# Kernel optimization log

Measured on AMD Instinct MI355X. Metric: run time of the kernel, lower is better.

Reference implementation:

```python
import jax, jax.numpy as jnp
import numpy as np

D = 1024          # d_model
DQ = D // 4       # embedding dim (d_model//4)
DH = D // 2       # head hidden (d_model//2)
P = 6             # n_digit_positions = max_int_digits + n_decimal_digits
NOPS, NPT = 9, 10
B, T = 8, 2048


def _ln(x, g, b, eps=1e-5):
    m = jnp.mean(x, axis=-1, keepdims=True)
    v = jnp.mean(jnp.square(x - m), axis=-1, keepdims=True)
    return (x - m) * jax.lax.rsqrt(v + eps) * g + b


def _xavier(key, shape):
    fan_in, fan_out = shape[-2], shape[-1]
    lim = np.sqrt(6.0 / (fan_in + fan_out))
    return jax.random.uniform(key, shape, jnp.float32, -lim, lim)


def setup_inputs() -> dict:
    key = jax.random.key(0)
    ks = jax.random.split(key, 20)
    inp = {
        'hidden': jax.random.normal(ks[0], (B, T, D), jnp.float32),
        'operation_type': jax.random.randint(ks[1], (B,), 0, NOPS),
        'param_type': jax.random.randint(ks[2], (B, T), 0, NPT),
        # embeddings (std=0.02 like the torch init)
        'op_embed': 0.02 * jax.random.normal(ks[3], (NOPS, DQ), jnp.float32),
        'pt_embed': 0.02 * jax.random.normal(ks[4], (NPT, DQ), jnp.float32),
        'pos_embed': 0.02 * jax.random.normal(ks[5], (P, DQ), jnp.float32),
        # context_proj: Linear(D + D//2 -> D) + LayerNorm(D)
        'ctx_w': _xavier(ks[6], (D + D // 2, D)),
        'ctx_b': jnp.zeros((D,), jnp.float32),
        'ctx_g': jnp.ones((D,), jnp.float32),
        'ctx_beta': jnp.zeros((D,), jnp.float32),
        # sign_head: Linear(D->DH), LN(DH), Linear(DH->3)
        'sign_w1': _xavier(ks[7], (D, DH)),
        'sign_b1': jnp.zeros((DH,), jnp.float32),
        'sign_g': jnp.ones((DH,), jnp.float32),
        'sign_beta': jnp.zeros((DH,), jnp.float32),
        'sign_w2': _xavier(ks[8], (DH, 3)),
        'sign_b2': jnp.zeros((3,), jnp.float32),
        # digit heads stacked over positions: Linear(D+DQ->DH), LN(DH), Linear(DH->10)
        'dig_w1': _xavier(ks[9], (P, D + DQ, DH)),
        'dig_b1': jnp.zeros((P, DH), jnp.float32),
        'dig_g': jnp.ones((P, DH), jnp.float32),
        'dig_beta': jnp.zeros((P, DH), jnp.float32),
        'dig_w2': _xavier(ks[10], (P, DH, 10)),
        'dig_b2': jnp.zeros((P, 10), jnp.float32),
        'aux_w1': _xavier(ks[11], (D, DH)),
        'aux_b1': jnp.zeros((DH,), jnp.float32),
        'aux_w2': _xavier(ks[12], (DH, 1)),
        'aux_b2': jnp.zeros((1,), jnp.float32),
    }
    return inp


def reference(hidden, operation_type, param_type, op_embed, pt_embed, pos_embed,
              ctx_w, ctx_b, ctx_g, ctx_beta,
              sign_w1, sign_b1, sign_g, sign_beta, sign_w2, sign_b2,
              dig_w1, dig_b1, dig_g, dig_beta, dig_w2, dig_b2,
              aux_w1, aux_b1, aux_w2, aux_b2):
    b, t, d = hidden.shape
    gelu = lambda x: jax.nn.gelu(x, approximate=False)  # torch nn.GELU default

    op_emb = jnp.broadcast_to(op_embed[operation_type][:, None, :], (b, t, DQ))
    pm_emb = pt_embed[param_type]                       # [B,T,DQ]
    ctx_in = jnp.concatenate([hidden, op_emb, pm_emb], axis=-1)  # [B,T,1.5D]
    context = gelu(_ln(ctx_in @ ctx_w + ctx_b, ctx_g, ctx_beta))  # [B,T,D]

    sh = gelu(_ln(context @ sign_w1 + sign_b1, sign_g, sign_beta))
    sign_logits = sh @ sign_w2 + sign_b2                # [B,T,3]

    # digit heads, vectorized over position. concat(context, pos_emb[p]) @ W1
    # == context @ W1[:, :D] + pos_emb[p] @ W1[:, D:]
    h = (jnp.einsum('btd,pdh->btph', context, dig_w1[:, :D, :])
         + jnp.einsum('pq,pqh->ph', pos_embed, dig_w1[:, D:, :])
         + dig_b1)                                      # [B,T,P,DH]
    h = gelu(_ln(h, dig_g, dig_beta))
    digit_logits = jnp.einsum('btph,pho->btpo', h, dig_w2) + dig_b2  # [B,T,P,10]

    aux_value = gelu(context @ aux_w1 + aux_b1) @ aux_w2 + aux_b2    # [B,T,1]

    return sign_logits, digit_logits, aux_value
```

## Files before the change

kernel.cpp:

```cpp
#include <hip/hip_runtime.h>
#include <hip/hip_bf16.h>

typedef unsigned short u16;
typedef __attribute__((ext_vector_type(8))) __bf16 bf16x8;
typedef __attribute__((ext_vector_type(4))) float f32x4;

typedef __attribute__((address_space(1))) const void GVoid;
typedef __attribute__((address_space(3))) void LVoid;

__device__ __forceinline__ void async_load16(const u16* g, u16* l) {
    __builtin_amdgcn_global_load_lds((GVoid*)g, (LVoid*)l, 16, 0, 0);
}

__device__ __forceinline__ float bf2f(u16 u) {
    union { unsigned i; float f; } v; v.i = ((unsigned)u) << 16; return v.f;
}
__device__ __forceinline__ u16 f2bf(float f) {
    union { float f; unsigned i; } v; v.f = f;
    unsigned r = (v.i + 0x7FFFu + ((v.i >> 16) & 1u)) >> 16;
    return (u16)r;
}
__device__ __forceinline__ float gelu_f(float x) {
    float t = x * fmaf(0.0356774081f, x * x, 0.7978845608f);
    float e = __expf(2.0f * t);
    float r = 1.0f / (e + 1.0f);
    return x - x * r;
}

#define OP_E   0
#define PT_E   2304
#define POS_E  4864
#define CTX_B  6400
#define CTX_G  7424
#define CTX_BE 8448
#define S_B1   9472
#define S_G    9984
#define S_BE   10496
#define S_B2   11008
#define D_G    11012
#define D_BE   14084
#define D_B2   17156
#define A_B1   17216
#define A_B2   17728

struct SmallTab {
    const float* src[15];
    int off[15];
    int cnt[15];
};

__global__ __launch_bounds__(256) void convert_small(SmallTab tab, u16* __restrict__ dst)
{
    int idx = blockIdx.x * 256 + threadIdx.x;
#pragma unroll
    for (int e = 0; e < 15; ++e) {
        if (idx < tab.cnt[e]) {
            dst[tab.off[e] + idx] = f2bf(tab.src[e][idx]);
            return;
        }
        idx -= tab.cnt[e];
    }
}

__global__ __launch_bounds__(256) void transpose_all(
    const float* __restrict__ ctx_w, const float* __restrict__ sign_w1,
    const float* __restrict__ aux_w1, const float* __restrict__ dig_w1,
    u16* __restrict__ ctxWt, u16* __restrict__ BtAll)
{
    __shared__ u16 tl[32][33];
    int z = blockIdx.z;
    const float* src; u16* dst; size_t srcOff = 0; int srcLd, cols;
    if (z == 8) { src = ctx_w; dst = ctxWt; srcLd = 1024; cols = 1024; }
    else {
        srcLd = 512; cols = 512;
        if (z == 0) src = sign_w1;
        else if (z == 1) src = aux_w1;
        else { src = dig_w1; srcOff = (size_t)(z - 2) * 1280 * 512; }
        dst = BtAll + (size_t)z * 512 * 1024;
    }
    int n0 = blockIdx.x * 32;
    if (n0 >= cols) return;
    int k0 = blockIdx.y * 32;
    int t = threadIdx.x;
    int r = t >> 3;
    int c4 = (t & 7) * 4;
    float4 v = *(const float4*)&src[srcOff + (size_t)(k0 + r) * srcLd + n0 + c4];
    tl[r][c4 + 0] = f2bf(v.x); tl[r][c4 + 1] = f2bf(v.y);
    tl[r][c4 + 2] = f2bf(v.z); tl[r][c4 + 3] = f2bf(v.w);
    __syncthreads();
    ushort4 o;
    o.x = tl[c4 + 0][r]; o.y = tl[c4 + 1][r]; o.z = tl[c4 + 2][r]; o.w = tl[c4 + 3][r];
    *(ushort4*)&dst[(size_t)(n0 + r) * 1024 + k0 + c4] = o;
}

__global__ __launch_bounds__(256) void precompute_bias(
    const float* __restrict__ ctx_w, const float* __restrict__ dig_w1,
    const float* __restrict__ op_embed, const float* __restrict__ pt_embed,
    const float* __restrict__ pos_embed, const float* __restrict__ dig_b1,
    const int* __restrict__ op_type,
    float* __restrict__ E_op, float* __restrict__ P_pt, float* __restrict__ dbias)
{
    int idx = blockIdx.x * 256 + threadIdx.x;
    if (idx < 8192) {
        int b = idx >> 10, n = idx & 1023;
        const float* e = op_embed + op_type[b] * 256;
        float s = 0.f;
        for (int q = 0; q < 256; ++q)
            s += e[q] * ctx_w[(size_t)(1024 + q) * 1024 + n];
        E_op[idx] = s;
    } else if (idx < 18432) {
        int i = idx - 8192;
        int v = i >> 10, n = i & 1023;
        const float* e = pt_embed + v * 256;
        float s = 0.f;
        for (int q = 0; q < 256; ++q)
            s += e[q] * ctx_w[(size_t)(1280 + q) * 1024 + n];
        P_pt[i] = s;
    } else if (idx < 21504) {
        int i = idx - 18432;
        int p = i >> 9, h = i & 511;
        const float* e = pos_embed + p * 256;
        float s = dig_b1[p * 512 + h];
        for (int q = 0; q < 256; ++q)
            s += e[q] * dig_w1[(size_t)p * 1280 * 512 + (size_t)(1024 + q) * 512 + h];
        dbias[i] = s;
    }
}

__global__ __launch_bounds__(256) void build_vec(
    const u16* __restrict__ csm, const float* __restrict__ dbias,
    float* __restrict__ biasAll, float* __restrict__ gammaAll,
    float* __restrict__ betaAll)
{
    int n = blockIdx.x * 256 + threadIdx.x;
    float bi, g, be;
    if (n < 512) {
        bi = bf2f(csm[S_B1 + n]); g = bf2f(csm[S_G + n]); be = bf2f(csm[S_BE + n]);
    } else if (n < 1024) {
        bi = bf2f(csm[A_B1 + n - 512]); g = 1.f; be = 0.f;
    } else {
        int h = n - 1024;
        bi = dbias[h]; g = bf2f(csm[D_G + h]); be = bf2f(csm[D_BE + h]);
    }
    biasAll[n] = bi; gammaAll[n] = g; betaAll[n] = be;
}

__global__ __launch_bounds__(256) void build_w2pad(
    const float* __restrict__ sign_w2, const float* __restrict__ dig_w2,
    const float* __restrict__ aux_w2, u16* __restrict__ W2pad)
{
    int idx = blockIdx.x * 256 + threadIdx.x;
    int row = idx >> 12, k = idx & 4095;
    int r = row >> 4, o = row & 15;
    float v = 0.f;
    if (r == 0) {
        if (o < 3 && k < 512) v = sign_w2[k * 3 + o];
    } else if (r == 7) {
        if (o == 0 && k >= 512 && k < 1024) v = aux_w2[k - 512];
    } else {
        int p = r - 1, lo = 1024 + p * 512;
        if (o < 10 && k >= lo && k < lo + 512) v = dig_w2[(size_t)p * 5120 + (k - lo) * 10 + o];
    }
    W2pad[idx] = f2bf(v);
}

__global__ __launch_bounds__(256) void gemm_bf16(
    const u16* __restrict__ A, const u16* __restrict__ Bt, u16* __restrict__ C,
    int M, int N, int K)
{
    __shared__ u16 As[128 * 32];
    __shared__ u16 Bs[128 * 32];
    const int tid = threadIdx.x;
    const int wid = tid >> 6, lane = tid & 63;
    const int m0 = blockIdx.x * 128, n0 = blockIdx.y * 128;
    const int mw = (wid >> 1) * 64, nw = (wid & 1) * 64;
    const int quad = lane >> 4, r16 = lane & 15;

    f32x4 acc[4][4] = {};

    const int srow = wid * 32 + (lane >> 2);
    const int scol = (lane & 3) * 8;
    const u16* gA = A + (size_t)(m0 + srow) * K + scol;
    const u16* gB = Bt + (size_t)(n0 + srow) * K + scol;
    u16* lA = As + wid * 32 * 32;
    u16* lB = Bs + wid * 32 * 32;

    for (int k0 = 0; k0 < K; k0 += 32) {
        async_load16(gA + k0, lA);
        async_load16(gA + k0 + (size_t)16 * K, lA + 16 * 32);
        async_load16(gB + k0, lB);
        async_load16(gB + k0 + (size_t)16 * K, lB + 16 * 32);
        __syncthreads();
        bf16x8 af[4], bw[4];
#pragma unroll
        for (int i = 0; i < 4; ++i)
            af[i] = *(const bf16x8*)&As[(mw + i * 16 + r16) * 32 + quad * 8];
#pragma unroll
        for (int j = 0; j < 4; ++j)
            bw[j] = *(const bf16x8*)&Bs[(nw + j * 16 + r16) * 32 + quad * 8];
#pragma unroll
        for (int i = 0; i < 4; ++i)
#pragma unroll
            for (int j = 0; j < 4; ++j)
                acc[i][j] = __builtin_amdgcn_mfma_f32_16x16x32_bf16(
                    af[i], bw[j], acc[i][j], 0, 0, 0);
        __syncthreads();
    }

#pragma unroll
    for (int i = 0; i < 4; ++i) {
#pragma unroll
        for (int j = 0; j < 4; ++j) {
            int col = n0 + nw + j * 16 + r16;
            size_t base = (size_t)(m0 + mw + i * 16 + quad * 4) * N + col;
#pragma unroll
            for (int r = 0; r < 4; ++r)
                C[base + (size_t)r * N] = f2bf(acc[i][j][r]);
        }
    }
}

__global__ __launch_bounds__(256) void gemm_f32a(
    const float* __restrict__ A, const u16* __restrict__ Bt, u16* __restrict__ C,
    int M, int N, int K)
{
    __shared__ u16 As[128 * 32];
    __shared__ u16 Bs[128 * 32];
    const int tid = threadIdx.x;
    const int wid = tid >> 6, lane = tid & 63;
    const int m0 = blockIdx.x * 128, n0 = blockIdx.y * 128;
    const int mw = (wid >> 1) * 64, nw = (wid & 1) * 64;
    const int quad = lane >> 4, r16 = lane & 15;

    f32x4 acc[4][4] = {};

    const int srow = wid * 32 + (lane >> 2);
    const int scol = (lane & 3) * 8;
    const u16* gB = Bt + (size_t)(n0 + srow) * K + scol;
    u16* lB = Bs + wid * 32 * 32;

    const int r0 = tid >> 2;
    const int c8 = (tid & 3) * 8;

    for (int k0 = 0; k0 < K; k0 += 32) {
        async_load16(gB + k0, lB);
        async_load16(gB + k0 + (size_t)16 * K, lB + 16 * 32);
        const float* p0 = &A[(size_t)(m0 + r0) * K + k0 + c8];
        const float* p1 = &A[(size_t)(m0 + 64 + r0) * K + k0 + c8];
        float4 x = *(const float4*)p0, y = *(const float4*)(p0 + 4);
        float4 u = *(const float4*)p1, w = *(const float4*)(p1 + 4);
        uint4 a0, a1;
        a0.x = f2bf(x.x) | ((unsigned)f2bf(x.y) << 16);
        a0.y = f2bf(x.z) | ((unsigned)f2bf(x.w) << 16);
        a0.z = f2bf(y.x) | ((unsigned)f2bf(y.y) << 16);
        a0.w = f2bf(y.z) | ((unsigned)f2bf(y.w) << 16);
        a1.x = f2bf(u.x) | ((unsigned)f2bf(u.y) << 16);
        a1.y = f2bf(u.z) | ((unsigned)f2bf(u.w) << 16);
        a1.z = f2bf(w.x) | ((unsigned)f2bf(w.y) << 16);
        a1.w = f2bf(w.z) | ((unsigned)f2bf(w.w) << 16);
        *(uint4*)&As[r0 * 32 + c8] = a0;
        *(uint4*)&As[(64 + r0) * 32 + c8] = a1;
        __syncthreads();

        bf16x8 af[4], bw[4];
#pragma unroll
        for (int i = 0; i < 4; ++i)
            af[i] = *(const bf16x8*)&As[(mw + i * 16 + r16) * 32 + quad * 8];
#pragma unroll
        for (int j = 0; j < 4; ++j)
            bw[j] = *(const bf16x8*)&Bs[(nw + j * 16 + r16) * 32 + quad * 8];
#pragma unroll
        for (int i = 0; i < 4; ++i)
#pragma unroll
            for (int j = 0; j < 4; ++j)
                acc[i][j] = __builtin_amdgcn_mfma_f32_16x16x32_bf16(
                    af[i], bw[j], acc[i][j], 0, 0, 0);
        __syncthreads();
    }

#pragma unroll
    for (int i = 0; i < 4; ++i) {
#pragma unroll
        for (int j = 0; j < 4; ++j) {
            int col = n0 + nw + j * 16 + r16;
            size_t base = (size_t)(m0 + mw + i * 16 + quad * 4) * N + col;
#pragma unroll
            for (int r = 0; r < 4; ++r)
                C[base + (size_t)r * N] = f2bf(acc[i][j][r]);
        }
    }
}

__global__ __launch_bounds__(256) void ln_ctx_kernel(
    const u16* __restrict__ pre, const float* __restrict__ E_op,
    const float* __restrict__ P_pt, const int* __restrict__ ptype,
    const u16* __restrict__ csm, u16* __restrict__ ctx, int tokOff)
{
    __shared__ float red[8];
    int local = blockIdx.x;
    int token = tokOff + local;
    int b = token >> 11;
    int pt = ptype[token];
    int tid = threadIdx.x;
    int c = tid * 4;
    int wid = tid >> 6, lane = tid & 63;

    ushort4 xp = *(const ushort4*)&pre[(size_t)local * 1024 + c];
    float4 eo = *(const float4*)&E_op[b * 1024 + c];
    float4 pp = *(const float4*)&P_pt[pt * 1024 + c];
    ushort4 cb4 = *(const ushort4*)&csm[CTX_B + c];
    float x[4];
    x[0] = bf2f(xp.x) + eo.x + pp.x + bf2f(cb4.x);
    x[1] = bf2f(xp.y) + eo.y + pp.y + bf2f(cb4.y);
    x[2] = bf2f(xp.z) + eo.z + pp.z + bf2f(cb4.z);
    x[3] = bf2f(xp.w) + eo.w + pp.w + bf2f(cb4.w);

    float s = x[0] + x[1] + x[2] + x[3];
    float s2 = x[0]*x[0] + x[1]*x[1] + x[2]*x[2] + x[3]*x[3];
    for (int off = 32; off; off >>= 1) { s += __shfl_xor(s, off); s2 += __shfl_xor(s2, off); }
    if (lane == 0) { red[wid] = s; red[4 + wid] = s2; }
    __syncthreads();
    s  = red[0] + red[1] + red[2] + red[3];
    s2 = red[4] + red[5] + red[6] + red[7];
    float mean = s * (1.f / 1024.f);
    float var = fmaxf(s2 * (1.f / 1024.f) - mean * mean, 0.f);
    float rs = rsqrtf(var + 1e-5f);

    ushort4 g4 = *(const ushort4*)&csm[CTX_G + c];
    ushort4 b4 = *(const ushort4*)&csm[CTX_BE + c];
    ushort4 o;
    o.x = f2bf(gelu_f((x[0] - mean) * rs * bf2f(g4.x) + bf2f(b4.x)));
    o.y = f2bf(gelu_f((x[1] - mean) * rs * bf2f(g4.y) + bf2f(b4.y)));
    o.z = f2bf(gelu_f((x[2] - mean) * rs * bf2f(g4.z) + bf2f(b4.z)));
    o.w = f2bf(gelu_f((x[3] - mean) * rs * bf2f(g4.w) + bf2f(b4.w)));
    *(ushort4*)&ctx[(size_t)token * 1024 + c] = o;
}

__global__ __launch_bounds__(256) void ln_stats(
    const u16* __restrict__ hp, const float* __restrict__ biasAll,
    float2* __restrict__ stats, int Rh)
{
    int wid = threadIdx.x >> 6, lane = threadIdx.x & 63;
    int idx = blockIdx.x * 4 + wid;
    int token = idx >> 3, s = idx & 7;
    const u16* row = hp + (size_t)token * 4096 + s * 512 + lane * 8;
    ushort4 a = ((const ushort4*)row)[0];
    ushort4 b = ((const ushort4*)row)[1];
    u16 xr[8]; *(ushort4*)&xr[0] = a; *(ushort4*)&xr[4] = b;
    const float* bi = biasAll + s * 512 + lane * 8;
    float4 b0 = *(const float4*)bi, b1 = *(const float4*)(bi + 4);
    float bb[8] = {b0.x, b0.y, b0.z, b0.w, b1.x, b1.y, b1.z, b1.w};
    float sm = 0.f, s2 = 0.f;
#pragma unroll
    for (int j = 0; j < 8; ++j) {
        float v = bf2f(xr[j]) + bb[j];
        sm += v; s2 += v * v;
    }
    for (int off = 32; off; off >>= 1) { sm += __shfl_xor(sm, off); s2 += __shfl_xor(s2, off); }
    if (lane == 0) {
        float mean = sm * (1.f / 512.f);
        float var = fmaxf(s2 * (1.f / 512.f) - mean * mean, 0.f);
        float2 st = make_float2(mean, rsqrtf(var + 1e-5f));
        if (s == 1) st = make_float2(0.f, 1.f);
        stats[idx] = st;
    }
}

__global__ __launch_bounds__(256) void gemm_final(
    const u16* __restrict__ A, const u16* __restrict__ W2pad,
    const float* __restrict__ biasAll, const float* __restrict__ gammaAll,
    const float* __restrict__ betaAll, const float2* __restrict__ stats,
    float* __restrict__ out_pre, int Rh)
{
    __shared__ u16 As[128 * 32];
    __shared__ u16 Bs[128 * 32];
    const int tid = threadIdx.x;
    const int wid = tid >> 6, lane = tid & 63;
    const int m0 = blockIdx.x * 128;
    const int ks = blockIdx.y, kbase = ks * 1024;
    const int mw = (wid >> 1) * 64, nw = (wid & 1) * 64;
    const int quad = lane >> 4, r16 = lane & 15;

    f32x4 acc[4][4] = {};

    const int srow = wid * 32 + (lane >> 2);
    const int scol = (lane & 3) * 8;
    const u16* gB = W2pad + (size_t)srow * 4096 + kbase + scol;
    u16* lB = Bs + wid * 32 * 32;

    const int r0 = tid >> 2;
    const int c8 = (tid & 3) * 8;

    for (int k0 = 0; k0 < 1024; k0 += 32) {
        async_load16(gB + k0, lB);
        async_load16(gB + k0 + (size_t)16 * 4096, lB + 16 * 32);
        int kk = kbase + k0 + c8;
        int sl = kk >> 9;
        float4 bi0 = *(const float4*)&biasAll[kk], bi1 = *(const float4*)&biasAll[kk + 4];
        float4 g0 = *(const float4*)&gammaAll[kk], g1 = *(const float4*)&gammaAll[kk + 4];
        float4 be0 = *(const float4*)&betaAll[kk], be1 = *(const float4*)&betaAll[kk + 4];
        float bb[8] = {bi0.x, bi0.y, bi0.z, bi0.w, bi1.x, bi1.y, bi1.z, bi1.w};
        float gg[8] = {g0.x, g0.y, g0.z, g0.w, g1.x, g1.y, g1.z, g1.w};
        float bt[8] = {be0.x, be0.y, be0.z, be0.w, be1.x, be1.y, be1.z, be1.w};
#pragma unroll
        for (int h = 0; h < 2; ++h) {
            int row = m0 + r0 + h * 64;
            const u16* ap = A + (size_t)row * 4096 + kk;
            ushort4 xa = ((const ushort4*)ap)[0];
            ushort4 xb = ((const ushort4*)ap)[1];
            u16 xr[8]; *(ushort4*)&xr[0] = xa; *(ushort4*)&xr[4] = xb;
            float2 st = stats[row * 8 + sl];
            u16 o[8];
#pragma unroll
            for (int j = 0; j < 8; ++j) {
                float v = (bf2f(xr[j]) + bb[j] - st.x) * st.y * gg[j] + bt[j];
                o[j] = f2bf(gelu_f(v));
            }
            *(uint4*)&As[(h * 64 + r0) * 32 + c8] = *(const uint4*)&o[0];
        }
        __syncthreads();

        bf16x8 af[4], bw[4];
#pragma unroll
        for (int i = 0; i < 4; ++i)
            af[i] = *(const bf16x8*)&As[(mw + i * 16 + r16) * 32 + quad * 8];
#pragma unroll
        for (int j = 0; j < 4; ++j)
            bw[j] = *(const bf16x8*)&Bs[(nw + j * 16 + r16) * 32 + quad * 8];
#pragma unroll
        for (int i = 0; i < 4; ++i)
#pragma unroll
            for (int j = 0; j < 4; ++j)
                acc[i][j] = __builtin_amdgcn_mfma_f32_16x16x32_bf16(
                    af[i], bw[j], acc[i][j], 0, 0, 0);
        __syncthreads();
    }

    float* op = out_pre + (size_t)ks * Rh * 128;
#pragma unroll
    for (int i = 0; i < 4; ++i) {
#pragma unroll
        for (int j = 0; j < 4; ++j) {
            int col = nw + j * 16 + r16;
            size_t base = (size_t)(m0 + mw + i * 16 + quad * 4) * 128 + col;
#pragma unroll
            for (int r = 0; r < 4; ++r)
                op[base + (size_t)r * 128] = acc[i][j][r];
        }
    }
}

__global__ __launch_bounds__(256) void gather_out(
    const float* __restrict__ out_pre, const u16* __restrict__ csm,
    float* __restrict__ out, int tokOff, int Rh)
{
    int idx = blockIdx.x * 256 + threadIdx.x;
    if (idx >= Rh * 64) return;
    int local = idx >> 6;
    int c = idx & 63;
    int token = tokOff + local;
    size_t P = (size_t)Rh * 128;
    size_t base = (size_t)local * 128;
    int col;
    if (c < 3) col = c;
    else if (c == 63) col = 7 * 16;
    else { int d = c - 3; int p = d / 10; col = (p + 1) * 16 + (d - p * 10); }
    float v = out_pre[base + col] + out_pre[P + base + col]
            + out_pre[2 * P + base + col] + out_pre[3 * P + base + col];
    if (c < 3) {
        out[(size_t)token * 3 + c] = v + bf2f(csm[S_B2 + c]);
    } else if (c == 63) {
        out[1032192 + (size_t)token] = v + bf2f(csm[A_B2]);
    } else {
        int d = c - 3;
        int p = d / 10, o = d - p * 10;
        out[49152 + ((size_t)token * 6 + p) * 10 + o] = v + bf2f(csm[D_B2 + p * 10 + o]);
    }
}

extern "C" void kernel_launch(void* const* d_in, const int* in_sizes, int n_in,
                              void* d_out, int out_size, void* d_ws, size_t ws_size,
                              hipStream_t stream) {
    const float* hidden    = (const float*)d_in[0];
    const int*   op_type   = (const int*)d_in[1];
    const int*   pt_type   = (const int*)d_in[2];
    const float* op_embed  = (const float*)d_in[3];
    const float* pt_embed  = (const float*)d_in[4];
    const float* pos_embed = (const float*)d_in[5];
    const float* ctx_w     = (const float*)d_in[6];
    const float* sign_w1   = (const float*)d_in[10];
    const float* sign_w2   = (const float*)d_in[14];
    const float* dig_w1    = (const float*)d_in[16];
    const float* dig_b1    = (const float*)d_in[17];
    const float* dig_w2    = (const float*)d_in[20];
    const float* aux_w1    = (const float*)d_in[22];
    const float* aux_w2    = (const float*)d_in[24];

    char* ws = (char*)d_ws;
    u16*    ctxWt    = (u16*)(ws + 0);
    u16*    BtAll    = (u16*)(ws + 2097152);
    float*  E_op     = (float*)(ws + 10485760);
    float*  P_pt     = (float*)(ws + 10518528);
    float*  dbias    = (float*)(ws + 10559488);
    u16*    csm      = (u16*)(ws + 10571776);
    float*  biasAll  = (float*)(ws + 10637312);
    float*  gammaAll = (float*)(ws + 10653696);
    float*  betaAll  = (float*)(ws + 10670080);
    float2* stats    = (float2*)(ws + 10686464);
    u16*    context  = (u16*)(ws + 11735040);
    u16*    scratch  = (u16*)(ws + 45289472);
    u16*    W2pad    = ctxWt;
    size_t S = (ws_size > 45289472) ? ws_size - 45289472 : 0;

    int Rc = 16384;
    while ((size_t)Rc * 2048 > S && Rc > 128) Rc >>= 1;
    int Rh = 16384;
    while ((size_t)Rh * 8192 > S && Rh > 128) Rh >>= 1;

    float* out = (float*)d_out;

    SmallTab tab;
    const float* srcs[15] = { op_embed, pt_embed, pos_embed,
                              (const float*)d_in[7], (const float*)d_in[8], (const float*)d_in[9],
                              (const float*)d_in[11], (const float*)d_in[12], (const float*)d_in[13],
                              (const float*)d_in[15],
                              (const float*)d_in[18], (const float*)d_in[19], (const float*)d_in[21],
                              (const float*)d_in[23], (const float*)d_in[25] };
    const int offs[15] = { OP_E, PT_E, POS_E, CTX_B, CTX_G, CTX_BE,
                           S_B1, S_G, S_BE, S_B2,
                           D_G, D_BE, D_B2, A_B1, A_B2 };
    const int cnts[15] = { 2304, 2560, 1536, 1024, 1024, 1024,
                           512, 512, 512, 3,
                           3072, 3072, 60, 512, 1 };
    for (int i = 0; i < 15; ++i) { tab.src[i] = srcs[i]; tab.off[i] = offs[i]; tab.cnt[i] = cnts[i]; }
    convert_small<<<70, 256, 0, stream>>>(tab, csm);

    transpose_all<<<dim3(32, 32, 9), 256, 0, stream>>>(
        ctx_w, sign_w1, aux_w1, dig_w1, ctxWt, BtAll);
    precompute_bias<<<84, 256, 0, stream>>>(
        ctx_w, dig_w1, op_embed, pt_embed, pos_embed, dig_b1, op_type,
        E_op, P_pt, dbias);
    build_vec<<<16, 256, 0, stream>>>(csm, dbias, biasAll, gammaAll, betaAll);

    for (int t0 = 0; t0 < 16384; t0 += Rc) {
        gemm_f32a<<<dim3(Rc / 128, 8), 256, 0, stream>>>(
            hidden + (size_t)t0 * 1024, ctxWt, scratch, Rc, 1024, 1024);
        ln_ctx_kernel<<<Rc, 256, 0, stream>>>(
            scratch, E_op, P_pt, pt_type, csm, context, t0);
    }

    build_w2pad<<<2048, 256, 0, stream>>>(sign_w2, dig_w2, aux_w2, W2pad);

    for (int t0 = 0; t0 < 16384; t0 += Rh) {
        gemm_bf16<<<dim3(Rh / 128, 32), 256, 0, stream>>>(
            context + (size_t)t0 * 1024, BtAll, scratch, Rh, 4096, 1024);
        ln_stats<<<Rh * 2, 256, 0, stream>>>(scratch, biasAll, stats, Rh);
        float* out_pre = (float*)(context + (size_t)t0 * 1024);
        gemm_final<<<dim3(Rh / 128, 4), 256, 0, stream>>>(
            scratch, W2pad, biasAll, gammaAll, betaAll, stats, out_pre, Rh);
        gather_out<<<(Rh * 64 + 255) / 256, 256, 0, stream>>>(
            out_pre, csm, out, t0, Rh);
    }
}
```

Baseline: 568.7 us.

## Replace head GEMM with 256x256 double-buffered, phase-interleaved MFMA kernel

Replaces the simple 128x128 single-buffered head GEMM with a 512-thread, 256x256-tile kernel that uses 128KB of LDS, a double-buffered K=64 pipeline, XOR-swizzled LDS layout, and four compute phases, each interleaved with async global-to-LDS loads and barriers. It also adds a grid swizzle for L2 locality and raises MFMA priority with setprio. The aim is to hide load latency behind MFMA work and raise arithmetic intensity in the largest GEMM (16384x4096x1024). Costs: hardcoded N=4096 and K=1024, a minimum chunk of 256 rows, and a single block per CU because of the LDS size.

```diff
diff --git a/kernel.cpp b/kernel.cpp
--- a/kernel.cpp
+++ b/kernel.cpp
@@ -164,58 +164,122 @@
     W2pad[idx] = f2bf(v);
 }
 
-__global__ __launch_bounds__(256) void gemm_bf16(
+__global__ __launch_bounds__(512) void gemm_head_8ph(
     const u16* __restrict__ A, const u16* __restrict__ Bt, u16* __restrict__ C,
-    int M, int N, int K)
-{
-    __shared__ u16 As[128 * 32];
-    __shared__ u16 Bs[128 * 32];
+    int M)
+{
+    __shared__ u16 smem[65536];
     const int tid = threadIdx.x;
     const int wid = tid >> 6, lane = tid & 63;
-    const int m0 = blockIdx.x * 128, n0 = blockIdx.y * 128;
-    const int mw = (wid >> 1) * 64, nw = (wid & 1) * 64;
     const int quad = lane >> 4, r16 = lane & 15;
-
-    f32x4 acc[4][4] = {};
-
-    const int srow = wid * 32 + (lane >> 2);
-    const int scol = (lane & 3) * 8;
-    const u16* gA = A + (size_t)(m0 + srow) * K + scol;
-    const u16* gB = Bt + (size_t)(n0 + srow) * K + scol;
-    u16* lA = As + wid * 32 * 32;
-    u16* lB = Bs + wid * 32 * 32;
-
-    for (int k0 = 0; k0 < K; k0 += 32) {
-        async_load16(gA + k0, lA);
-        async_load16(gA + k0 + (size_t)16 * K, lA + 16 * 32);
-        async_load16(gB + k0, lB);
-        async_load16(gB + k0 + (size_t)16 * K, lB + 16 * 32);
-        __syncthreads();
-        bf16x8 af[4], bw[4];
-#pragma unroll
-        for (int i = 0; i < 4; ++i)
-            af[i] = *(const bf16x8*)&As[(mw + i * 16 + r16) * 32 + quad * 8];
-#pragma unroll
-        for (int j = 0; j < 4; ++j)
-            bw[j] = *(const bf16x8*)&Bs[(nw + j * 16 + r16) * 32 + quad * 8];
-#pragma unroll
-        for (int i = 0; i < 4; ++i)
-#pragma unroll
-            for (int j = 0; j < 4; ++j)
-                acc[i][j] = __builtin_amdgcn_mfma_f32_16x16x32_bf16(
-                    af[i], bw[j], acc[i][j], 0, 0, 0);
-        __syncthreads();
-    }
-
-#pragma unroll
-    for (int i = 0; i < 4; ++i) {
-#pragma unroll
-        for (int j = 0; j < 4; ++j) {
-            int col = n0 + nw + j * 16 + r16;
-            size_t base = (size_t)(m0 + mw + i * 16 + quad * 4) * N + col;
+    const int wm = wid >> 2, wn = wid & 3;
+
+    const int Mtiles = M >> 8;
+    int flat = blockIdx.x + blockIdx.y * gridDim.x;
+    int cpx = (Mtiles * 16) >> 3;
+    int swz = (flat & 7) * cpx + (flat >> 3);
+    int bm = swz % Mtiles, bn = swz / Mtiles;
+    const int m0 = bm << 8, n0 = bn << 8;
+
+    const int rb = tid >> 3;
+    const int cx = ((tid & 7) ^ (rb & 7)) * 8;
+    const u16* gA = A + (size_t)(m0 + rb) * 1024 + cx;
+    const u16* gB = Bt + (size_t)(n0 + rb) * 1024 + cx;
+
+#define STAGE(arr, h, tt) do { \
+        u16* _d = smem + ((((tt) & 1) * 2 + (arr)) * 2 + (h)) * 8192 + wid * 512; \
+        const u16* _s = ((arr) ? gB : gA) + (size_t)((h) * 128) * 1024 + (tt) * 64; \
+        async_load16(_s, _d); \
+        async_load16(_s + (size_t)64 * 1024, _d + 4096); \
+    } while (0)
+
+    STAGE(0, 0, 0); STAGE(0, 1, 0); STAGE(1, 0, 0); STAGE(1, 1, 0);
+    STAGE(0, 0, 1); STAGE(0, 1, 1); STAGE(1, 0, 1);
+    asm volatile("s_waitcnt vmcnt(6)" ::: "memory");
+    asm volatile("s_barrier" ::: "memory");
+
+    f32x4 acc[8][4] = {};
+    const int kx0 = ((quad) ^ (r16 & 7)) * 8;
+    const int kx1 = ((4 + quad) ^ (r16 & 7)) * 8;
+
+#define QUAD(MF0, NF0) \
+        _Pragma("unroll") \
+        for (int ks = 0; ks < 2; ++ks) \
+            _Pragma("unroll") \
+            for (int mi = 0; mi < 4; ++mi) \
+                _Pragma("unroll") \
+                for (int nj = 0; nj < 2; ++nj) \
+                    acc[(MF0) + mi][(NF0) + nj] = \
+                        __builtin_amdgcn_mfma_f32_16x16x32_bf16( \
+                            afr[(MF0) + mi][ks], bfr[(NF0) + nj][ks], \
+                            acc[(MF0) + mi][(NF0) + nj], 0, 0, 0);
+
+    for (int t = 0; t < 16; ++t) {
+        const int cur = t & 1;
+        const u16* sA = smem + cur * 32768 + wm * 8192 + r16 * 64;
+        const u16* sB = smem + cur * 32768 + 16384 + (wn >> 1) * 8192
+                        + ((wn & 1) * 64 + r16) * 64;
+
+        if (t + 1 < 16) STAGE(1, 1, t + 1);
+        bf16x8 afr[8][2], bfr[4][2];
+#pragma unroll
+        for (int mf = 0; mf < 8; ++mf) {
+            afr[mf][0] = *(const bf16x8*)&sA[mf * 1024 + kx0];
+            afr[mf][1] = *(const bf16x8*)&sA[mf * 1024 + kx1];
+        }
+#pragma unroll
+        for (int nf = 0; nf < 4; ++nf) {
+            bfr[nf][0] = *(const bf16x8*)&sB[nf * 1024 + kx0];
+            bfr[nf][1] = *(const bf16x8*)&sB[nf * 1024 + kx1];
+        }
+        __builtin_amdgcn_s_setprio(1);
+        QUAD(0, 0)
+        __builtin_amdgcn_s_setprio(0);
+        asm volatile("s_waitcnt lgkmcnt(0)" ::: "memory");
+        __builtin_amdgcn_sched_barrier(0);
+        asm volatile("s_barrier" ::: "memory");
+        __builtin_amdgcn_sched_barrier(0);
+
+        if (t + 2 < 16) STAGE(0, 0, t + 2);
+        __builtin_amdgcn_sched_barrier(0);
+        __builtin_amdgcn_s_setprio(1);
+        QUAD(0, 2)
+        __builtin_amdgcn_s_setprio(0);
+        __builtin_amdgcn_sched_barrier(0);
+        asm volatile("s_barrier" ::: "memory");
+        __builtin_amdgcn_sched_barrier(0);
+
+        if (t + 2 < 16) STAGE(0, 1, t + 2);
+        __builtin_amdgcn_sched_barrier(0);
+        __builtin_amdgcn_s_setprio(1);
+        QUAD(4, 0)
+        __builtin_amdgcn_s_setprio(0);
+        __builtin_amdgcn_sched_barrier(0);
+        asm volatile("s_barrier" ::: "memory");
+        __builtin_amdgcn_sched_barrier(0);
+
+        if (t + 2 < 16) STAGE(1, 0, t + 2);
+        __builtin_amdgcn_sched_barrier(0);
+        __builtin_amdgcn_s_setprio(1);
+        QUAD(4, 2)
+        __builtin_amdgcn_s_setprio(0);
+        __builtin_amdgcn_sched_barrier(0);
+        if (t < 14)       asm volatile("s_waitcnt vmcnt(6)" ::: "memory");
+        else if (t == 14) asm volatile("s_waitcnt vmcnt(0)" ::: "memory");
+        asm volatile("s_barrier" ::: "memory");
+    }
+#undef QUAD
+#undef STAGE
+
+#pragma unroll
+    for (int mf = 0; mf < 8; ++mf) {
+#pragma unroll
+        for (int nf = 0; nf < 4; ++nf) {
+            size_t base = (size_t)(m0 + wm * 128 + mf * 16 + quad * 4) * 4096
+                          + n0 + wn * 64 + nf * 16 + r16;
 #pragma unroll
             for (int r = 0; r < 4; ++r)
-                C[base + (size_t)r * N] = f2bf(acc[i][j][r]);
+                C[base + (size_t)r * 4096] = f2bf(acc[mf][nf][r]);
         }
     }
 }
@@ -515,7 +579,7 @@
     int Rc = 16384;
     while ((size_t)Rc * 2048 > S && Rc > 128) Rc >>= 1;
     int Rh = 16384;
-    while ((size_t)Rh * 8192 > S && Rh > 128) Rh >>= 1;
+    while ((size_t)Rh * 8192 > S && Rh > 256) Rh >>= 1;
 
     float* out = (float*)d_out;
 
@@ -552,8 +616,8 @@
     build_w2pad<<<2048, 256, 0, stream>>>(sign_w2, dig_w2, aux_w2, W2pad);
 
     for (int t0 = 0; t0 < 16384; t0 += Rh) {
-        gemm_bf16<<<dim3(Rh / 128, 32), 256, 0, stream>>>(
-            context + (size_t)t0 * 1024, BtAll, scratch, Rh, 4096, 1024);
+        gemm_head_8ph<<<dim3(Rh / 256, 16), 512, 0, stream>>>(
+            context + (size_t)t0 * 1024, BtAll, scratch, Rh);
         ln_stats<<<Rh * 2, 256, 0, stream>>>(scratch, biasAll, stats, Rh);
         float* out_pre = (float*)(context + (size_t)t0 * 1024);
         gemm_final<<<dim3(Rh / 128, 4), 256, 0, stream>>>(
```

Measured after the change: 522.3 us. 1.09x faster.
